# Kernel optimization log

Measured on AMD Instinct MI355X. Metric: run time of the kernel, lower is better.

## Reference

```python
import jax, jax.numpy as jnp
import numpy as np

DIM = 1024
NUM_HEADS = 16
NUM_GROUPS = 8


def setup_inputs() -> dict:
    key = jax.random.key(0)
    k1, k2, k3, k4 = jax.random.split(key, 4)
    B, L = 4, 4096
    x = jax.random.normal(k1, (B, L, DIM), dtype=jnp.float32)
    # torch Linear weights: [out_features, in_features]
    w_qkv = jax.random.normal(k2, (3 * DIM, DIM), dtype=jnp.float32) * (DIM ** -0.5)
    w_out = jax.random.normal(k3, (DIM, DIM), dtype=jnp.float32) * (DIM ** -0.5)
    b_out = jax.random.normal(k4, (DIM,), dtype=jnp.float32) * 0.01
    return {"x": x, "w_qkv": w_qkv, "w_out": w_out, "b_out": b_out}


def reference(x, w_qkv, w_out, b_out):
    B, L, D = x.shape
    H, G = NUM_HEADS, NUM_GROUPS
    dh = D // H
    lg = L // G  # block length per group
    # fused QKV projection (no bias)
    qkv = x @ w_qkv.T  # [B, L, 3D]
    qkv = qkv.reshape(B, L, 3, H, dh)
    qkv = jnp.transpose(qkv, (2, 0, 3, 1, 4))  # [3, B, H, L, dh]
    q, k, v = qkv[0], qkv[1], qkv[2]
    # group sequence into G blocks of length lg; attention within each block
    q = q.reshape(B, H, G, lg, dh)
    k = k.reshape(B, H, G, lg, dh)
    v = v.reshape(B, H, G, lg, dh)
    scale = dh ** -0.5
    scores = jnp.einsum('bhgld,bhgmd->bhglm', q, k) * scale  # [B,H,G,lg,lg]
    attn = jax.nn.softmax(scores, axis=-1)
    out = jnp.einsum('bhglm,bhgmd->bhgld', attn, v)  # [B,H,G,lg,dh]
    # 'b h g l d -> b (g l) (h d)'
    out = jnp.transpose(out, (0, 2, 3, 1, 4)).reshape(B, L, D)
    return out @ w_out.T + b_out
```

## Files before the change

kernel.cpp:

```cpp
#include <hip/hip_runtime.h>
#include <hip/hip_bf16.h>
#include <stdint.h>

typedef __bf16 bf16_t;
typedef __bf16 bf16x8 __attribute__((ext_vector_type(8)));
typedef float floatx4 __attribute__((ext_vector_type(4)));

#define MFMA_16x16x32_BF16(a, b, c) __builtin_amdgcn_mfma_f32_16x16x32_bf16((a), (b), (c), 0, 0, 0)

__device__ __forceinline__ void gload_lds16(const bf16_t* g, bf16_t* lds_base) {
  __builtin_amdgcn_global_load_lds(
      (const __attribute__((address_space(1))) void*)g,
      (__attribute__((address_space(3))) void*)lds_base, 16, 0, 0);
}

__global__ __launch_bounds__(256)
void f32_to_bf16_kernel(const float* __restrict__ in, bf16_t* __restrict__ out, int n8)
{
  for (int i = blockIdx.x * 256 + threadIdx.x; i < n8; i += gridDim.x * 256) {
    const float* p = in + (size_t)i * 8;
    floatx4 f0 = *(const floatx4*)p;
    floatx4 f1 = *(const floatx4*)(p + 4);
    bf16x8 r;
#pragma unroll
    for (int j = 0; j < 4; j++) { r[j] = (bf16_t)f0[j]; r[j + 4] = (bf16_t)f1[j]; }
    *(bf16x8*)(out + (size_t)i * 8) = r;
  }
}

template <typename TOUT, bool BIAS>
__global__ __launch_bounds__(512, 1)
void gemm_bt256(const bf16_t* __restrict__ A, const bf16_t* __restrict__ B,
                const float* __restrict__ bias, TOUT* __restrict__ C,
                int M, int N, int K)
{
  __shared__ bf16_t S[65536];
  const int t = threadIdx.x;
  const int lane = t & 63, wave = t >> 6;
  const int quad = lane >> 4, l15 = lane & 15;
  const int wm = wave >> 2, wn = wave & 3;

  const int cpx = gridDim.x >> 3;
  const int obid = blockIdx.x;
  const int bid = (obid & 7) * cpx + (obid >> 3);
  const int nbx = N >> 8;
  const int bx = bid % nbx, by = bid / nbx;
  const int m0 = by * 256, n0 = bx * 256;

  uint32_t aoff[4], boff[4];
  bf16_t* asd[4]; bf16_t* bsd[4];
#pragma unroll
  for (int j = 0; j < 4; j++) {
    const uint32_t o = (uint32_t)(j * 512 + t) * 16u;
    const uint32_t u = o ^ (((o >> 7) & 7u) << 4);
    const uint32_t row = u >> 7, colb = u & 127u;
    aoff[j] = (uint32_t)(m0 + row) * (uint32_t)(K * 2) + colb;
    boff[j] = (uint32_t)(n0 + row) * (uint32_t)(K * 2) + colb;
    asd[j] = S + j * 4096 + wave * 512;
    bsd[j] = S + 32768 + j * 4096 + wave * 512;
  }

  const uint32_t sw = (uint32_t)((l15 & 7) << 4);
  const uint32_t ce0 = (((uint32_t)(quad * 16)) ^ sw) >> 1;
  const uint32_t ce1 = ce0 ^ 32u;
  const bf16_t* lraA0 = S + (wm * 128 + l15) * 64 + ce0;
  const bf16_t* lraA1 = S + (wm * 128 + l15) * 64 + ce1;
  const bf16_t* lraB0 = S + 32768 + (wn * 64 + l15) * 64 + ce0;
  const bf16_t* lraB1 = S + 32768 + (wn * 64 + l15) * 64 + ce1;

  floatx4 acc[8][4] = {};

  const int NT = K >> 6;
#pragma unroll
  for (int j = 0; j < 4; j++) gload_lds16((const bf16_t*)((const char*)A + aoff[j]), asd[j]);
#pragma unroll
  for (int j = 0; j < 4; j++) gload_lds16((const bf16_t*)((const char*)B + boff[j]), bsd[j]);
#pragma unroll
  for (int j = 0; j < 4; j++) gload_lds16((const bf16_t*)((const char*)A + aoff[j] + 128), asd[j] + 16384);
#pragma unroll
  for (int j = 0; j < 4; j++) gload_lds16((const bf16_t*)((const char*)B + boff[j] + 128), bsd[j] + 16384);

  for (int kt = 0; kt < NT; kt++) {
    const int bo = (kt & 1) * 16384;
    if (kt < NT - 1) asm volatile("s_waitcnt vmcnt(8)" ::: "memory");
    else             asm volatile("s_waitcnt vmcnt(0)" ::: "memory");
    __builtin_amdgcn_s_barrier();
    __builtin_amdgcn_sched_barrier(0);

    bf16x8 af[4][2], bA[2][2], bB[2][2];
#pragma unroll
    for (int mi = 0; mi < 4; mi++) {
      af[mi][0] = *(const bf16x8*)(lraA0 + bo + mi * 1024);
      af[mi][1] = *(const bf16x8*)(lraA1 + bo + mi * 1024);
    }
#pragma unroll
    for (int ni = 0; ni < 2; ni++) {
      bA[ni][0] = *(const bf16x8*)(lraB0 + bo + ni * 1024);
      bA[ni][1] = *(const bf16x8*)(lraB1 + bo + ni * 1024);
    }
    __builtin_amdgcn_s_setprio(1);
#pragma unroll
    for (int mi = 0; mi < 4; mi++)
#pragma unroll
      for (int ni = 0; ni < 2; ni++) {
        acc[mi][ni] = MFMA_16x16x32_BF16(af[mi][0], bA[ni][0], acc[mi][ni]);
        acc[mi][ni] = MFMA_16x16x32_BF16(af[mi][1], bA[ni][1], acc[mi][ni]);
      }
    __builtin_amdgcn_s_setprio(0);
#pragma unroll
    for (int ni = 0; ni < 2; ni++) {
      bB[ni][0] = *(const bf16x8*)(lraB0 + bo + (ni + 2) * 1024);
      bB[ni][1] = *(const bf16x8*)(lraB1 + bo + (ni + 2) * 1024);
    }
    __builtin_amdgcn_s_setprio(1);
#pragma unroll
    for (int mi = 0; mi < 4; mi++)
#pragma unroll
      for (int ni = 0; ni < 2; ni++) {
        acc[mi][ni + 2] = MFMA_16x16x32_BF16(af[mi][0], bB[ni][0], acc[mi][ni + 2]);
        acc[mi][ni + 2] = MFMA_16x16x32_BF16(af[mi][1], bB[ni][1], acc[mi][ni + 2]);
      }
    __builtin_amdgcn_s_setprio(0);
#pragma unroll
    for (int mi = 0; mi < 4; mi++) {
      af[mi][0] = *(const bf16x8*)(lraA0 + bo + (mi + 4) * 1024);
      af[mi][1] = *(const bf16x8*)(lraA1 + bo + (mi + 4) * 1024);
    }
    __builtin_amdgcn_s_setprio(1);
#pragma unroll
    for (int mi = 0; mi < 4; mi++)
#pragma unroll
      for (int ni = 0; ni < 2; ni++) {
        acc[mi + 4][ni + 2] = MFMA_16x16x32_BF16(af[mi][0], bB[ni][0], acc[mi + 4][ni + 2]);
        acc[mi + 4][ni + 2] = MFMA_16x16x32_BF16(af[mi][1], bB[ni][1], acc[mi + 4][ni + 2]);
      }
    __builtin_amdgcn_s_setprio(0);
    __builtin_amdgcn_sched_barrier(0);
    __builtin_amdgcn_s_barrier();
    __builtin_amdgcn_sched_barrier(0);
    if (kt + 2 < NT) {
      const uint32_t kadv = (uint32_t)((kt + 2) * 128);
#pragma unroll
      for (int j = 0; j < 4; j++)
        gload_lds16((const bf16_t*)((const char*)A + aoff[j] + kadv), asd[j] + bo);
#pragma unroll
      for (int j = 0; j < 4; j++)
        gload_lds16((const bf16_t*)((const char*)B + boff[j] + kadv), bsd[j] + bo);
    }
    __builtin_amdgcn_s_setprio(1);
#pragma unroll
    for (int mi = 0; mi < 4; mi++)
#pragma unroll
      for (int ni = 0; ni < 2; ni++) {
        acc[mi + 4][ni] = MFMA_16x16x32_BF16(af[mi][0], bA[ni][0], acc[mi + 4][ni]);
        acc[mi + 4][ni] = MFMA_16x16x32_BF16(af[mi][1], bA[ni][1], acc[mi + 4][ni]);
      }
    __builtin_amdgcn_s_setprio(0);
  }

#pragma unroll
  for (int ni = 0; ni < 4; ni++) {
    const int col = n0 + wn * 64 + ni * 16 + l15;
    const float bv = BIAS ? bias[col] : 0.0f;
#pragma unroll
    for (int mi = 0; mi < 8; mi++) {
      const size_t rbase = (size_t)(m0 + wm * 128 + mi * 16 + quad * 4) * N + col;
#pragma unroll
      for (int r = 0; r < 4; r++)
        C[rbase + (size_t)r * N] = (TOUT)(acc[mi][ni][r] + bv);
    }
  }
}

__global__ __launch_bounds__(256)
void attn_kernel(const bf16_t* __restrict__ qkv, bf16_t* __restrict__ out)
{
  constexpr int VS = 72;
  __shared__ bf16_t Ks[64 * VS];
  __shared__ bf16_t Vt[64 * VS];
  __shared__ bf16_t Ps[4][16 * VS];

  const int h     = blockIdx.x & 15;
  const int qtile = blockIdx.x >> 4;

  const int t = threadIdx.x;
  const int wave = t >> 6, lane = t & 63;
  const int quad = lane >> 4, l15 = lane & 15;

  const int qrow0 = qtile * 256 + wave * 64;
  const int krow0 = (qtile >> 1) * 512;
  const int qcol = h * 64;
  const int kcol = 1024 + h * 64;
  const int vcol = 2048 + h * 64;

  bf16x8 qf[4][2];
#pragma unroll
  for (int mi = 0; mi < 4; mi++)
#pragma unroll
    for (int kb = 0; kb < 2; kb++)
      qf[mi][kb] = *(const bf16x8*)(qkv + (size_t)(qrow0 + mi * 16 + l15) * 3072 + qcol + kb * 32 + quad * 8);

  floatx4 o[4][4] = {};
  float plsum[4][4] = {};

  const float SCL = 0.125f * 1.44269504088896f;

  const bf16_t* kg0 = qkv + (size_t)(krow0 + (t >> 3)) * 3072 + kcol + (t & 7) * 8;
  const bf16_t* kg1 = qkv + (size_t)(krow0 + 32 + (t >> 3)) * 3072 + kcol + (t & 7) * 8;
  const bf16_t* vg0 = qkv + (size_t)(krow0 + (t & 63)) * 3072 + vcol + (t >> 6) * 8;
  const bf16_t* vg1 = qkv + (size_t)(krow0 + (t & 63)) * 3072 + vcol + ((t >> 6) + 4) * 8;
  bf16_t* ksd0 = Ks + (t >> 3) * VS + (t & 7) * 8;
  bf16_t* ksd1 = Ks + ((t >> 3) + 32) * VS + (t & 7) * 8;
  bf16_t* vtd0 = Vt + (t >> 6) * 8 * VS + (t & 63);
  bf16_t* vtd1 = Vt + ((t >> 6) + 4) * 8 * VS + (t & 63);

  bf16x8 kreg0 = *(const bf16x8*)kg0;
  bf16x8 kreg1 = *(const bf16x8*)kg1;
  bf16x8 vreg0 = *(const bf16x8*)vg0;
  bf16x8 vreg1 = *(const bf16x8*)vg1;

  for (int it = 0; it < 8; it++) {
    __syncthreads();
    *(bf16x8*)ksd0 = kreg0;
    *(bf16x8*)ksd1 = kreg1;
#pragma unroll
    for (int j = 0; j < 8; j++) { vtd0[j * VS] = vreg0[j]; vtd1[j * VS] = vreg1[j]; }
    __syncthreads();

    if (it < 7) {
      const size_t off = (size_t)(it + 1) * 64 * 3072;
      kreg0 = *(const bf16x8*)(kg0 + off);
      kreg1 = *(const bf16x8*)(kg1 + off);
      vreg0 = *(const bf16x8*)(vg0 + off);
      vreg1 = *(const bf16x8*)(vg1 + off);
    }

    bf16x8 kf[4][2], vf[4][2];
#pragma unroll
    for (int ni = 0; ni < 4; ni++)
#pragma unroll
      for (int kb = 0; kb < 2; kb++) {
        kf[ni][kb] = *(const bf16x8*)(Ks + (ni * 16 + l15) * VS + kb * 32 + quad * 8);
        vf[ni][kb] = *(const bf16x8*)(Vt + (ni * 16 + l15) * VS + kb * 32 + quad * 8);
      }

#pragma unroll
    for (int mi = 0; mi < 4; mi++) {
      floatx4 s[4] = {};
      __builtin_amdgcn_s_setprio(1);
#pragma unroll
      for (int ni = 0; ni < 4; ni++) {
        s[ni] = MFMA_16x16x32_BF16(qf[mi][0], kf[ni][0], s[ni]);
        s[ni] = MFMA_16x16x32_BF16(qf[mi][1], kf[ni][1], s[ni]);
      }
      __builtin_amdgcn_s_setprio(0);
#pragma unroll
      for (int r = 0; r < 4; r++) {
        float ps = 0.0f;
#pragma unroll
        for (int ni = 0; ni < 4; ni++) {
          const float p = exp2f(s[ni][r] * SCL);
          ps += p;
          Ps[wave][(quad * 4 + r) * VS + ni * 16 + l15] = (bf16_t)p;
        }
        plsum[mi][r] += ps;
      }
      bf16x8 pf0 = *(const bf16x8*)(Ps[wave] + l15 * VS + quad * 8);
      bf16x8 pf1 = *(const bf16x8*)(Ps[wave] + l15 * VS + 32 + quad * 8);
      __builtin_amdgcn_s_setprio(1);
#pragma unroll
      for (int ni = 0; ni < 4; ni++) {
        o[mi][ni] = MFMA_16x16x32_BF16(pf0, vf[ni][0], o[mi][ni]);
        o[mi][ni] = MFMA_16x16x32_BF16(pf1, vf[ni][1], o[mi][ni]);
      }
      __builtin_amdgcn_s_setprio(0);
    }
  }

#pragma unroll
  for (int mi = 0; mi < 4; mi++)
#pragma unroll
    for (int r = 0; r < 4; r++) {
      float tot = plsum[mi][r];
#pragma unroll
      for (int off = 1; off < 16; off <<= 1)
        tot += __shfl_xor(tot, off, 64);
      const float inv = 1.0f / tot;
      const size_t rbase = (size_t)(qrow0 + mi * 16 + quad * 4 + r) * 1024 + h * 64 + l15;
#pragma unroll
      for (int ni = 0; ni < 4; ni++)
        out[rbase + ni * 16] = (bf16_t)(o[mi][ni][r] * inv);
    }
}

extern "C" void kernel_launch(void* const* d_in, const int* in_sizes, int n_in,
                              void* d_out, int out_size, void* d_ws, size_t ws_size,
                              hipStream_t stream)
{
  const float* x     = (const float*)d_in[0];
  const float* w_qkv = (const float*)d_in[1];
  const float* w_out = (const float*)d_in[2];
  const float* b_out = (const float*)d_in[3];
  float* out = (float*)d_out;

  const size_t WQ = (size_t)3072 * 1024, WO = (size_t)1024 * 1024;
  bf16_t* wq_b = (bf16_t*)d_ws;
  bf16_t* wo_b = wq_b + WQ;

  int rows = 16384;
  while ((size_t)rows * 10240 + (WQ + WO) * 2 > ws_size && rows > 512) rows >>= 1;
  const int nchunk = 16384 / rows;

  bf16_t* qkv_c = wo_b + WO;
  bf16_t* att_c = qkv_c + (size_t)rows * 3072;
  bf16_t* x_c   = att_c + (size_t)rows * 1024;

  f32_to_bf16_kernel<<<1536, 256, 0, stream>>>(w_qkv, wq_b, (int)(WQ / 8));
  f32_to_bf16_kernel<<<512, 256, 0, stream>>>(w_out, wo_b, (int)(WO / 8));

  for (int c = 0; c < nchunk; c++) {
    const float* xc = x + (size_t)c * rows * 1024;
    float* outc = out + (size_t)c * rows * 1024;
    f32_to_bf16_kernel<<<2048, 256, 0, stream>>>(xc, x_c, rows * 128);
    gemm_bt256<bf16_t, false><<<dim3((3072 / 256) * (rows / 256)), 512, 0, stream>>>(
        x_c, wq_b, nullptr, qkv_c, rows, 3072, 1024);
    attn_kernel<<<dim3(16 * (rows / 256)), 256, 0, stream>>>(qkv_c, att_c);
    gemm_bt256<float, true><<<dim3((1024 / 256) * (rows / 256)), 512, 0, stream>>>(
        att_c, wo_b, b_out, outc, rows, 1024, 1024);
  }
}
```

Before: 368.7 us.

## Stage bf16 GEMM epilogue through LDS and transpose QK^T in attention

For bf16 outputs, the GEMM epilogue now writes accumulators into a swizzled LDS tile and reads them back as 16-byte rows, replacing scattered 2-byte global stores with coalesced vector stores. In the attention kernel, the QK^T MFMA operands are swapped so each lane holds scores for one query row. This lets P be written to LDS as bf16x4 vectors and reduces the softmax row-sum reduction from a 16-lane shuffle tree per row to two shuffles plus a broadcast. The costs are an extra __syncthreads and reuse of the GEMM's LDS buffer S in the epilogue.

```diff
diff --git a/kernel.cpp b/kernel.cpp
--- a/kernel.cpp
+++ b/kernel.cpp
@@ -3,6 +3,7 @@
 #include <stdint.h>
 
 typedef __bf16 bf16_t;
+typedef __bf16 bf16x4 __attribute__((ext_vector_type(4)));
 typedef __bf16 bf16x8 __attribute__((ext_vector_type(8)));
 typedef float floatx4 __attribute__((ext_vector_type(4)));
 
@@ -158,16 +159,42 @@
     __builtin_amdgcn_s_setprio(0);
   }
 
-#pragma unroll
-  for (int ni = 0; ni < 4; ni++) {
-    const int col = n0 + wn * 64 + ni * 16 + l15;
-    const float bv = BIAS ? bias[col] : 0.0f;
+  if constexpr (sizeof(TOUT) == 2) {
+    __syncthreads();
+    bf16_t* Sw = S + wave * 1024;
 #pragma unroll
     for (int mi = 0; mi < 8; mi++) {
-      const size_t rbase = (size_t)(m0 + wm * 128 + mi * 16 + quad * 4) * N + col;
-#pragma unroll
-      for (int r = 0; r < 4; r++)
-        C[rbase + (size_t)r * N] = (TOUT)(acc[mi][ni][r] + bv);
+#pragma unroll
+      for (int ni = 0; ni < 4; ni++) {
+        const int col = ((ni ^ quad) & 3) * 16 + l15;
+        const float bv = BIAS ? bias[n0 + wn * 64 + ni * 16 + l15] : 0.0f;
+#pragma unroll
+        for (int r = 0; r < 4; r++)
+          Sw[(quad * 4 + r) * 64 + col] = (bf16_t)(acc[mi][ni][r] + bv);
+      }
+#pragma unroll
+      for (int c = 0; c < 2; c++) {
+        const int idx = c * 64 + lane;
+        const int row = idx >> 3, cg = idx & 7;
+        const int scol = (cg * 8) ^ (((row >> 2) & 3) << 4);
+        bf16x8 vrow = *(const bf16x8*)(Sw + row * 64 + scol);
+        bf16_t* dst = (bf16_t*)C + (size_t)(m0 + wm * 128 + mi * 16 + row) * N
+                      + (n0 + wn * 64 + cg * 8);
+        *(bf16x8*)dst = vrow;
+      }
+    }
+  } else {
+#pragma unroll
+    for (int ni = 0; ni < 4; ni++) {
+      const int col = n0 + wn * 64 + ni * 16 + l15;
+      const float bv = BIAS ? bias[col] : 0.0f;
+#pragma unroll
+      for (int mi = 0; mi < 8; mi++) {
+        const size_t rbase = (size_t)(m0 + wm * 128 + mi * 16 + quad * 4) * N + col;
+#pragma unroll
+        for (int r = 0; r < 4; r++)
+          C[rbase + (size_t)r * N] = (TOUT)(acc[mi][ni][r] + bv);
+      }
     }
   }
 }
@@ -201,7 +228,7 @@
       qf[mi][kb] = *(const bf16x8*)(qkv + (size_t)(qrow0 + mi * 16 + l15) * 3072 + qcol + kb * 32 + quad * 8);
 
   floatx4 o[4][4] = {};
-  float plsum[4][4] = {};
+  float plsum[4] = {};
 
   const float SCL = 0.125f * 1.44269504088896f;
 
@@ -250,21 +277,23 @@
       __builtin_amdgcn_s_setprio(1);
 #pragma unroll
       for (int ni = 0; ni < 4; ni++) {
-        s[ni] = MFMA_16x16x32_BF16(qf[mi][0], kf[ni][0], s[ni]);
-        s[ni] = MFMA_16x16x32_BF16(qf[mi][1], kf[ni][1], s[ni]);
+        s[ni] = MFMA_16x16x32_BF16(kf[ni][0], qf[mi][0], s[ni]);
+        s[ni] = MFMA_16x16x32_BF16(kf[ni][1], qf[mi][1], s[ni]);
       }
       __builtin_amdgcn_s_setprio(0);
-#pragma unroll
-      for (int r = 0; r < 4; r++) {
-        float ps = 0.0f;
-#pragma unroll
-        for (int ni = 0; ni < 4; ni++) {
+      float ps = 0.0f;
+#pragma unroll
+      for (int ni = 0; ni < 4; ni++) {
+        bf16x4 w;
+#pragma unroll
+        for (int r = 0; r < 4; r++) {
           const float p = exp2f(s[ni][r] * SCL);
           ps += p;
-          Ps[wave][(quad * 4 + r) * VS + ni * 16 + l15] = (bf16_t)p;
+          w[r] = (bf16_t)p;
         }
-        plsum[mi][r] += ps;
-      }
+        *(bf16x4*)(Ps[wave] + l15 * VS + ni * 16 + quad * 4) = w;
+      }
+      plsum[mi] += ps;
       bf16x8 pf0 = *(const bf16x8*)(Ps[wave] + l15 * VS + quad * 8);
       bf16x8 pf1 = *(const bf16x8*)(Ps[wave] + l15 * VS + 32 + quad * 8);
       __builtin_amdgcn_s_setprio(1);
@@ -278,19 +307,20 @@
   }
 
 #pragma unroll
-  for (int mi = 0; mi < 4; mi++)
+  for (int mi = 0; mi < 4; mi++) {
+    float tot = plsum[mi];
+    tot += __shfl_xor(tot, 16, 64);
+    tot += __shfl_xor(tot, 32, 64);
+    const float inv = 1.0f / tot;
 #pragma unroll
     for (int r = 0; r < 4; r++) {
-      float tot = plsum[mi][r];
-#pragma unroll
-      for (int off = 1; off < 16; off <<= 1)
-        tot += __shfl_xor(tot, off, 64);
-      const float inv = 1.0f / tot;
+      const float invr = __shfl(inv, quad * 4 + r, 16);
       const size_t rbase = (size_t)(qrow0 + mi * 16 + quad * 4 + r) * 1024 + h * 64 + l15;
 #pragma unroll
       for (int ni = 0; ni < 4; ni++)
-        out[rbase + ni * 16] = (bf16_t)(o[mi][ni][r] * inv);
-    }
+        out[rbase + ni * 16] = (bf16_t)(o[mi][ni][r] * invr);
+    }
+  }
 }
 
 extern "C" void kernel_launch(void* const* d_in, const int* in_sizes, int n_in,
```

After: 362.8 us. No clear change (-1.6%).
